# Kernel optimization log

Measured on AMD Instinct MI355X. Metric: run time of the kernel, lower is better.

The kernel has to match this reference:

```python
import jax, jax.numpy as jnp
import numpy as np

MODES1 = 64
MODES2 = 64

def _c(t):
    # real view (..., 2) -> complex
    return jax.lax.complex(t[..., 0], t[..., 1])

def _contract_tt(xf, a, b, c, d):
    # xf: (B, Cin, m1, m2) complex
    # a: (1, Cout, r1, 2), b: (r1, Cin, r2, 2), c: (r2, m1, r3, 2), d: (r3, m2, 1, 2)
    ac = _c(a)[0]          # (Cout, r1)
    bc = _c(b)             # (r1, Cin, r2)
    cc = _c(c)             # (r2, m1, r3)
    dc = _c(d)[..., 0]     # (r3, m2)
    o1 = jnp.einsum('jxk,ky,bcxy->jbcxy', cc, dc, xf)   # (r2, B, Cin, m1, m2)
    return jnp.einsum('oi,icj,jbcxy->boxy', ac, bc, o1)  # (B, Cout, m1, m2)

def setup_inputs() -> dict:
    key = jax.random.key(0)
    ks = jax.random.split(key, 9)
    std = 0.02
    inp = {
        'x':  jax.random.normal(ks[0], (4, 128, 256, 256), dtype=jnp.float32),
        'a1': std * jax.random.normal(ks[1], (1, 128, 64, 2), dtype=jnp.float32),
        'b1': std * jax.random.normal(ks[2], (64, 128, 32, 2), dtype=jnp.float32),
        'c1': std * jax.random.normal(ks[3], (32, 64, 32, 2), dtype=jnp.float32),
        'd1': std * jax.random.normal(ks[4], (32, 64, 1, 2), dtype=jnp.float32),
        'a2': std * jax.random.normal(ks[5], (1, 128, 64, 2), dtype=jnp.float32),
        'b2': std * jax.random.normal(ks[6], (64, 128, 32, 2), dtype=jnp.float32),
        'c2': std * jax.random.normal(ks[7], (32, 64, 32, 2), dtype=jnp.float32),
        'd2': std * jax.random.normal(ks[8], (32, 64, 1, 2), dtype=jnp.float32),
    }
    return inp

def reference(x, a1, b1, c1, d1, a2, b2, c2, d2):
    B, Cin, H, W = x.shape
    Cout = a1.shape[1]
    x_ft = jnp.fft.rfft2(x)  # (B, Cin, H, W//2+1) complex64
    out1 = _contract_tt(x_ft[:, :, :MODES1, :MODES2], a1, b1, c1, d1)
    out2 = _contract_tt(x_ft[:, :, -MODES1:, :MODES2], a2, b2, c2, d2)
    out_ft = jnp.zeros((B, Cout, H, W // 2 + 1), dtype=x_ft.dtype)
    out_ft = out_ft.at[:, :, :MODES1, :MODES2].set(out1)
    out_ft = out_ft.at[:, :, -MODES1:, :MODES2].set(out2)
    return jnp.fft.irfft2(out_ft, s=(H, W))
```

## Files before the change

kernel.cpp:

```cpp
#include <hip/hip_runtime.h>
#include <math.h>


#define TWO_PI 6.28318530717958647692f

typedef __attribute__((ext_vector_type(8))) short short8v;
typedef __attribute__((ext_vector_type(4))) float float4v;

namespace {
constexpr size_t P_ = 32768;

constexpr size_t oYT = 0;
constexpr size_t oTA = 1048576;
constexpr size_t oXF = 16777216;
constexpr size_t oOF = 25165824;
constexpr size_t oBF = 33554432;
constexpr size_t oAF1 = 33587200;
constexpr size_t oAF2 = 33685504;
constexpr size_t oG  = 33792000;
constexpr size_t oEF = oG + 262144;
constexpr size_t WS_FLOATS = oG + 524288;
}

__device__ __forceinline__ unsigned short f2bf(float f) {
    unsigned int u = __float_as_uint(f);
    unsigned int r = (u + 0x7FFFu + ((u >> 16) & 1u)) >> 16;
    return (unsigned short)r;
}
__device__ __forceinline__ float bf2f(unsigned short b) {
    return __uint_as_float(((unsigned int)b) << 16);
}

__global__ __launch_bounds__(256) void k_prepTables(const float* __restrict__ a1,
                                                    const float* __restrict__ a2,
                                                    unsigned short* __restrict__ AF1,
                                                    unsigned short* __restrict__ AF2,
                                                    unsigned short* __restrict__ BF,
                                                    unsigned short* __restrict__ EF,
                                                    unsigned short* __restrict__ AFa) {
    int idx = blockIdx.x * 256 + threadIdx.x;
    if (idx < 196608) {
        int tbl = (idx >= 98304);
        int id = tbl ? (idx - 98304) : idx;
        int e = id & 7, lane = (id >> 3) & 63;
        int pl = id >> 15;
        float ang;
        if (!tbl) {
            int rt = (id >> 9) & 7, kc = (id >> 12) & 7;
            int r = rt * 16 + (lane & 15);
            int s = kc * 32 + 8 * (lane >> 4) + e;
            int kh = r + ((r >= 64) ? 128 : 0);
            int ph = (kh * s) & 255;
            ang = -TWO_PI * (float)ph / 256.0f;
        } else {
            int rt = (id >> 9) & 15, kc = (id >> 13) & 3;
            int r = rt * 16 + (lane & 15);
            int s = kc * 32 + 8 * (lane >> 4) + e;
            int kh = s + ((s >= 64) ? 128 : 0);
            int ph = (kh * r) & 255;
            ang = TWO_PI * (float)ph / 256.0f;
        }
        float sn, cs; sincosf(ang, &sn, &cs);
        float v = (pl == 0) ? cs : ((pl == 1) ? sn : -sn);
        (tbl ? AF2 : AF1)[id] = f2bf(v);
    } else if (idx < 229376) {
        int id = idx - 196608;
        int e = id & 7, lane = (id >> 3) & 63;
        int nt = (id >> 9) & 3, kc = (id >> 11) & 7;
        int pl = id >> 14;
        int kw = nt * 16 + (lane & 15);
        int w = kc * 32 + 8 * (lane >> 4) + e;
        int ph = (w * kw) & 255;
        float ang = -TWO_PI * (float)ph / 256.0f;
        float sn, cs; sincosf(ang, &sn, &cs);
        BF[id] = f2bf((pl == 0) ? cs : sn);
    } else if (idx < 262144) {
        int id = idx - 229376;
        int e = id & 7, lane = (id >> 3) & 63;
        int nt = (id >> 9) & 15, kc = (id >> 13) & 1, pl = id >> 14;
        int w = nt * 16 + (lane & 15);
        int kw = kc * 32 + 8 * (lane >> 4) + e;
        int ph = (kw * w) & 255;
        float ang = TWO_PI * (float)ph / 256.0f;
        float sn, cs; sincosf(ang, &sn, &cs);
        float sc = ((kw == 0) ? 1.0f : 2.0f) / 65536.0f;
        float v = (pl == 0) ? (sc * cs) : (-sc * sn);
        EF[id] = f2bf(v);
    } else {
        int id = idx - 262144;
        int e = id & 7, lane = (id >> 3) & 63;
        int rt = (id >> 9) & 7, kc = (id >> 12) & 1;
        int plreg = id >> 13;
        int reg = plreg / 3, pl = plreg % 3;
        int o = rt * 16 + (lane & 15);
        int i = kc * 32 + 8 * (lane >> 4) + e;
        const float* ap = reg ? a2 : a1;
        float ar = ap[(o * 64 + i) * 2 + 0];
        float ai = ap[(o * 64 + i) * 2 + 1];
        float v = (pl == 0) ? ar : ((pl == 1) ? ai : -ai);
        AFa[id] = f2bf(v);
    }
}

__global__ __launch_bounds__(256) void k_g(const float* __restrict__ c1, const float* __restrict__ d1,
                                           const float* __restrict__ c2, const float* __restrict__ d2,
                                           float2* __restrict__ G) {
    int idx = blockIdx.x * 256 + threadIdx.x;
    int r = idx >> 17;
    int rem = idx & 131071;
    int j = rem >> 12;
    int xy = rem & 4095;
    int xm = xy >> 6, ym = xy & 63;
    const float* cp = r ? c2 : c1;
    const float* dp = r ? d2 : d1;
    float sr = 0.f, si = 0.f;
    for (int kk = 0; kk < 32; ++kk) {
        float cr = cp[((j * 64 + xm) * 32 + kk) * 2 + 0];
        float ci = cp[((j * 64 + xm) * 32 + kk) * 2 + 1];
        float dr = dp[(kk * 64 + ym) * 2 + 0];
        float di = dp[(kk * 64 + ym) * 2 + 1];
        sr = fmaf(cr, dr, fmaf(-ci, di, sr));
        si = fmaf(cr, di, fmaf( ci, dr, si));
    }
    G[(size_t)(r * 32 + j) * 4096 + xy] = make_float2(sr, si);
}

__global__ __launch_bounds__(256) void k_prepBG(const float* __restrict__ b1, const float* __restrict__ b2,
                                                const float2* __restrict__ G,
                                                unsigned short* __restrict__ bA,
                                                unsigned short* __restrict__ gB) {
    size_t idx = (size_t)blockIdx.x * 256 + threadIdx.x;
    if (idx < 1048576) {
        int e     = idx & 7;
        int lane  = (idx >> 3) & 63;
        int c     = (idx >> 9) & 127;
        int itile = (idx >> 16) & 3;
        int reg   = (idx >> 18) & 1;
        int plane = (idx >> 19) & 1;
        int i = itile * 16 + (lane & 15);
        int j = 8 * (lane >> 4) + e;
        const float* bp = reg ? b2 : b1;
        float v = bp[((size_t)(i * 128 + c) * 32 + j) * 2 + plane];
        bA[idx] = f2bf(v);
    } else if (idx < 1048576 + 786432) {
        size_t i2 = idx - 1048576;
        int e     = i2 & 7;
        int lane  = (i2 >> 3) & 63;
        int ytile = (i2 >> 9) & 3;
        int x     = (i2 >> 11) & 63;
        int reg   = (i2 >> 17) & 1;
        int plane = (int)(i2 >> 18);
        int y = ytile * 16 + (lane & 15);
        int j = 8 * (lane >> 4) + e;
        float2 gv = G[(size_t)(reg * 32 + j) * 4096 + x * 64 + y];
        float v = (plane == 0) ? gv.x : ((plane == 1) ? gv.y : -gv.y);
        gB[i2] = f2bf(v);
    }
}

__global__ __launch_bounds__(256) void k_stage1m(const float* __restrict__ x,
                                                 const unsigned short* __restrict__ BF,
                                                 unsigned short* __restrict__ Yt) {
    __shared__ __align__(16) unsigned short es[8192];
    int t = threadIdx.x;
    int wave = t >> 6, lane = t & 63;
    size_t row0 = (size_t)blockIdx.x * 128 + (size_t)wave * 32;
    int colp = lane & 15, rowq = lane >> 4;
    const short8v* esv = (const short8v*)es;

    float4v accR[2][4], accI[2][4];
#pragma unroll
    for (int rt = 0; rt < 2; ++rt)
#pragma unroll
        for (int nt = 0; nt < 4; ++nt) {
            accR[rt][nt] = (float4v){0.f, 0.f, 0.f, 0.f};
            accI[rt][nt] = (float4v){0.f, 0.f, 0.f, 0.f};
        }

    const float* xb0 = x + (row0 + colp) * 256 + 8 * rowq;
    const float* xb1 = xb0 + 16 * 256;
    float4 nv[2][2];
    nv[0][0] = *(const float4*)(xb0);  nv[0][1] = *(const float4*)(xb0 + 4);
    nv[1][0] = *(const float4*)(xb1);  nv[1][1] = *(const float4*)(xb1 + 4);

    const float4* bf4 = (const float4*)BF;
    for (int ph = 0; ph < 4; ++ph) {
        __syncthreads();
        {
#pragma unroll
            for (int i = 0; i < 4; ++i) {
                int idx = t + 256 * i;
                int li  = idx & 63;
                int nt  = (idx >> 6) & 3;
                int kcl = (idx >> 8) & 1;
                int pl  = idx >> 9;
                ((float4*)es)[idx] = bf4[((size_t)(pl * 8 + ph * 2 + kcl) * 4 + nt) * 64 + li];
            }
        }
        __syncthreads();
        for (int kcl = 0; kcl < 2; ++kcl) {
            int kc = ph * 2 + kcl;
            short8v xh[2];
#pragma unroll
            for (int rt = 0; rt < 2; ++rt) {
                float4 v0 = nv[rt][0], v1 = nv[rt][1];
                float vv[8] = {v0.x, v0.y, v0.z, v0.w, v1.x, v1.y, v1.z, v1.w};
#pragma unroll
                for (int j = 0; j < 8; ++j) xh[rt][j] = (short)f2bf(vv[j]);
            }
            if (kc < 7) {
                nv[0][0] = *(const float4*)(xb0 + (kc + 1) * 32);
                nv[0][1] = *(const float4*)(xb0 + (kc + 1) * 32 + 4);
                nv[1][0] = *(const float4*)(xb1 + (kc + 1) * 32);
                nv[1][1] = *(const float4*)(xb1 + (kc + 1) * 32 + 4);
            }
#pragma unroll
            for (int nt = 0; nt < 4; ++nt) {
                short8v Bch = esv[((0 * 2 + kcl) * 4 + nt) * 64 + lane];
                short8v Bsh = esv[((1 * 2 + kcl) * 4 + nt) * 64 + lane];
#pragma unroll
                for (int rt = 0; rt < 2; ++rt) {
                    accR[rt][nt] = __builtin_amdgcn_mfma_f32_16x16x32_bf16(xh[rt], Bch, accR[rt][nt], 0, 0, 0);
                    accI[rt][nt] = __builtin_amdgcn_mfma_f32_16x16x32_bf16(xh[rt], Bsh, accI[rt][nt], 0, 0, 0);
                }
            }
        }
    }

    short* Yts = (short*)Yt;
    const size_t PLY = (size_t)32 * 32768 * 8;
#pragma unroll
    for (int rt = 0; rt < 2; ++rt) {
        size_t xrow0 = row0 + rt * 16 + rowq * 4;
        int h = (int)(xrow0 & 255), bc = (int)(xrow0 >> 8);
        size_t gbase = (size_t)(h >> 3) * 32768;
        int e0 = h & 7;
#pragma unroll
        for (int nt = 0; nt < 4; ++nt) {
            size_t p = (size_t)bc * 64 + nt * 16 + colp;
            size_t off = (gbase + p) * 8 + e0;
            float4v R = accR[rt][nt], I = accI[rt][nt];
            short rh[4], ih[4];
#pragma unroll
            for (int q = 0; q < 4; ++q) {
                rh[q] = (short)f2bf(R[q]);
                ih[q] = (short)f2bf(I[q]);
            }
            *(short4*)&Yts[0 * PLY + off] = make_short4(rh[0], rh[1], rh[2], rh[3]);
            *(short4*)&Yts[1 * PLY + off] = make_short4(ih[0], ih[1], ih[2], ih[3]);
        }
    }
}

template<int S, int RT_W>
__global__ __launch_bounds__(256) void k_cmfma(const unsigned short* __restrict__ AF,
                                               const unsigned short* __restrict__ Bt,
                                               unsigned int* __restrict__ XFh) {
    constexpr int KC = S / 32;
    constexpr int SG = S / 8;
    constexpr int RTOT = RT_W * 4;
    __shared__ __align__(16) unsigned short bs[2 * SG * 16 * 8];
    int t = threadIdx.x;
    int wave = t >> 6, lane = t & 63;
    int rt0 = wave * RT_W;
    int colp = lane & 15, rowq = lane >> 4;
    const short8v* AFv = (const short8v*)AF;
    const short8v* bsv = (const short8v*)bs;
    const size_t PLA = (size_t)KC * RTOT * 64;

    for (int pt = 0; pt < 4; ++pt) {
        int p0 = blockIdx.x * 64 + pt * 16;
        __syncthreads();
        {
            const float4* src = (const float4*)Bt;
            float4* dst = (float4*)bs;
            for (int e = t; e < 2 * SG * 16; e += 256) {
                int pl = e / (SG * 16); int rem = e - pl * (SG * 16);
                int g = rem >> 4, li = rem & 15;
                dst[e] = src[((size_t)pl * SG + g) * 32768 + p0 + li];
            }
        }
        __syncthreads();
        float4v accR[RT_W], accI[RT_W];
#pragma unroll
        for (int rt = 0; rt < RT_W; ++rt) {
            accR[rt] = (float4v){0.f, 0.f, 0.f, 0.f};
            accI[rt] = (float4v){0.f, 0.f, 0.f, 0.f};
        }
#pragma unroll
        for (int kc = 0; kc < KC; ++kc) {
            int gi = kc * 4 + rowq;
            short8v Brh = bsv[((0 * SG + gi) << 4) + colp];
            short8v Bih = bsv[((1 * SG + gi) << 4) + colp];
#pragma unroll
            for (int rt = 0; rt < RT_W; ++rt) {
                size_t ab = ((size_t)kc * RTOT + rt0 + rt) * 64 + lane;
                short8v Ac  = AFv[0 * PLA + ab];
                short8v As  = AFv[1 * PLA + ab];
                short8v Ans = AFv[2 * PLA + ab];
                float4v r_ = accR[rt];
                r_ = __builtin_amdgcn_mfma_f32_16x16x32_bf16(Ac,  Brh, r_, 0, 0, 0);
                r_ = __builtin_amdgcn_mfma_f32_16x16x32_bf16(Ans, Bih, r_, 0, 0, 0);
                accR[rt] = r_;
                float4v i_ = accI[rt];
                i_ = __builtin_amdgcn_mfma_f32_16x16x32_bf16(As, Brh, i_, 0, 0, 0);
                i_ = __builtin_amdgcn_mfma_f32_16x16x32_bf16(Ac, Bih, i_, 0, 0, 0);
                accI[rt] = i_;
            }
        }
#pragma unroll
        for (int rt = 0; rt < RT_W; ++rt) {
            int rbase = (rt0 + rt) * 16 + rowq * 4;
#pragma unroll
            for (int q = 0; q < 4; ++q) {
                unsigned int pw = (unsigned int)f2bf(accR[rt][q])
                                | ((unsigned int)f2bf(accI[rt][q]) << 16);
                XFh[(size_t)(rbase + q) * P_ + p0 + colp] = pw;
            }
        }
    }
}

__global__ __launch_bounds__(256) void k_contractA(const unsigned int* __restrict__ XFh,
                                                   const unsigned short* __restrict__ bA,
                                                   const unsigned short* __restrict__ gB,
                                                   unsigned short* __restrict__ tA) {
    __shared__ __align__(16) unsigned int xfs[4][128][16];
    int t = threadIdx.x;
    int k = blockIdx.x >> 2;
    int ytile = blockIdx.x & 3;
    int y0 = ytile << 4;
    int reg = (k >= 64) ? 1 : 0;
    int x = k & 63;
    int itile = t >> 6, lane = t & 63;
    int ylane = lane & 15, qg = lane >> 4;

    {
        const uint4* src = (const uint4*)XFh;
        uint4* dst = (uint4*)xfs;
        size_t kbase = ((size_t)k * 32768 + y0) >> 2;
#pragma unroll
        for (int i = 0; i < 8; ++i) {
            int e = t + 256 * i;
            int f4w = e & 3;
            int bc  = e >> 2;
            int b   = bc >> 7, c = bc & 127;
            dst[e] = src[kbase + (size_t)b * 2048 + (size_t)c * 16 + f4w];
        }
    }

    const short8v* gBv = (const short8v*)gB;
    short8v g_r  = gBv[(((size_t)(0 * 2 + reg) * 64 + x) * 4 + ytile) * 64 + lane];
    short8v g_i  = gBv[(((size_t)(1 * 2 + reg) * 64 + x) * 4 + ytile) * 64 + lane];
    short8v g_ni = gBv[(((size_t)(2 * 2 + reg) * 64 + x) * 4 + ytile) * 64 + lane];

    const short8v* bAv = (const short8v*)bA;
    size_t aR = (((size_t)(0 * 2 + reg) * 4 + itile) * 128) * 64 + lane;
    size_t aI = (((size_t)(1 * 2 + reg) * 4 + itile) * 128) * 64 + lane;

    float tr[4][4], ti[4][4];
#pragma unroll
    for (int q = 0; q < 4; ++q)
#pragma unroll
        for (int b = 0; b < 4; ++b) { tr[q][b] = 0.f; ti[q][b] = 0.f; }

    __syncthreads();

#pragma unroll 2
    for (int c = 0; c < 128; ++c) {
        short8v av = bAv[aR + (size_t)c * 64];
        short8v aw = bAv[aI + (size_t)c * 64];
        float4v z4 = {0.f, 0.f, 0.f, 0.f};
        float4v wr = __builtin_amdgcn_mfma_f32_16x16x32_bf16(av, g_r, z4, 0, 0, 0);
        wr = __builtin_amdgcn_mfma_f32_16x16x32_bf16(aw, g_ni, wr, 0, 0, 0);
        float4v wi = __builtin_amdgcn_mfma_f32_16x16x32_bf16(av, g_i, z4, 0, 0, 0);
        wi = __builtin_amdgcn_mfma_f32_16x16x32_bf16(aw, g_r, wi, 0, 0, 0);
#pragma unroll
        for (int b = 0; b < 4; ++b) {
            unsigned int xw = xfs[b][c][ylane];
            float xr = bf2f((unsigned short)(xw & 0xFFFFu));
            float xi = bf2f((unsigned short)(xw >> 16));
#pragma unroll
            for (int q = 0; q < 4; ++q) {
                tr[q][b] = fmaf(wr[q], xr, fmaf(-wi[q], xi, tr[q][b]));
                ti[q][b] = fmaf(wr[q], xi, fmaf( wi[q], xr, ti[q][b]));
            }
        }
    }

    short* tAs = (short*)tA;
    const size_t PLT = (size_t)8 * 32768 * 8;
    int gidx = itile * 2 + (qg >> 1);
    int e0 = (qg & 1) * 4;
#pragma unroll
    for (int b = 0; b < 4; ++b) {
        size_t col = (size_t)k * 256 + (size_t)b * 64 + y0 + ylane;
        size_t off = ((size_t)gidx * 32768 + col) * 8 + e0;
        short rh[4], ih[4];
#pragma unroll
        for (int q = 0; q < 4; ++q) {
            rh[q] = (short)f2bf(tr[q][b]);
            ih[q] = (short)f2bf(ti[q][b]);
        }
        *(short4*)&tAs[0 * PLT + off] = make_short4(rh[0], rh[1], rh[2], rh[3]);
        *(short4*)&tAs[1 * PLT + off] = make_short4(ih[0], ih[1], ih[2], ih[3]);
    }
}

__global__ __launch_bounds__(256) void k_amfma(const unsigned short* __restrict__ AFa,
                                               const unsigned short* __restrict__ tA,
                                               unsigned int* __restrict__ OFh) {
    constexpr int SG = 8;
    __shared__ __align__(16) unsigned short bs[2 * SG * 16 * 8];
    int t = threadIdx.x;
    int wave = t >> 6, lane = t & 63;
    int rt0 = wave * 2;
    int colp = lane & 15, rowq = lane >> 4;
    int k = blockIdx.x >> 2, b = blockIdx.x & 3;
    int reg = (k >= 64) ? 1 : 0;
    const short8v* AFv = (const short8v*)(AFa + (size_t)reg * 3 * 2 * 8 * 512);
    const size_t PLA = 2 * 8 * 64;
    const short8v* bsv = (const short8v*)bs;
    size_t p0 = (size_t)blockIdx.x * 64;

    for (int pt = 0; pt < 4; ++pt) {
        __syncthreads();
        {
            const float4* src = (const float4*)tA;
            float4* dst = (float4*)bs;
            int e = t;
            int pl = e >> 7; int rem = e & 127;
            int g = rem >> 4, li = rem & 15;
            dst[e] = src[((size_t)pl * SG + g) * 32768 + p0 + pt * 16 + li];
        }
        __syncthreads();
        float4v accR[2], accI[2];
#pragma unroll
        for (int rt = 0; rt < 2; ++rt) {
            accR[rt] = (float4v){0.f, 0.f, 0.f, 0.f};
            accI[rt] = (float4v){0.f, 0.f, 0.f, 0.f};
        }
#pragma unroll
        for (int kc = 0; kc < 2; ++kc) {
            int gi = kc * 4 + rowq;
            short8v Brh = bsv[((0 * SG + gi) << 4) + colp];
            short8v Bih = bsv[((1 * SG + gi) << 4) + colp];
#pragma unroll
            for (int rt = 0; rt < 2; ++rt) {
                size_t ab = ((size_t)kc * 8 + rt0 + rt) * 64 + lane;
                short8v Ar  = AFv[0 * PLA + ab];
                short8v Ai  = AFv[1 * PLA + ab];
                short8v Ani = AFv[2 * PLA + ab];
                float4v r_ = accR[rt];
                r_ = __builtin_amdgcn_mfma_f32_16x16x32_bf16(Ar,  Brh, r_, 0, 0, 0);
                r_ = __builtin_amdgcn_mfma_f32_16x16x32_bf16(Ani, Bih, r_, 0, 0, 0);
                accR[rt] = r_;
                float4v i_ = accI[rt];
                i_ = __builtin_amdgcn_mfma_f32_16x16x32_bf16(Ai, Brh, i_, 0, 0, 0);
                i_ = __builtin_amdgcn_mfma_f32_16x16x32_bf16(Ar, Bih, i_, 0, 0, 0);
                accI[rt] = i_;
            }
        }
        int m = pt * 16 + colp;
#pragma unroll
        for (int rt = 0; rt < 2; ++rt) {
            int o0 = (rt0 + rt) * 16 + rowq * 4;
#pragma unroll
            for (int q = 0; q < 4; ++q) {
                unsigned int pw = (unsigned int)f2bf(accR[rt][q])
                                | ((unsigned int)f2bf(accI[rt][q]) << 16);
                OFh[(size_t)k * 32768 + (size_t)b * 8192 + (size_t)(o0 + q) * 64 + m] = pw;
            }
        }
    }
}

__global__ __launch_bounds__(512) void k_ihinv(const unsigned short* __restrict__ AF2,
                                               const unsigned int* __restrict__ OFh,
                                               const unsigned short* __restrict__ EF,
                                               float* __restrict__ out) {
    constexpr int SG = 16, KC = 4, RTOT = 16;
    __shared__ __align__(16) unsigned short zs[2 * 256 * 64];
    __shared__ __align__(16) unsigned short bs[2 * SG * 16 * 8];
    int t = threadIdx.x;
    int wave = t >> 6, lane = t & 63;
    int colp = lane & 15, rowq = lane >> 4;
    int rt0 = wave * 2;
    int bo = blockIdx.x;
    size_t p0 = (size_t)bo * 64;
    const short8v* AFv = (const short8v*)AF2;
    const short8v* bsv = (const short8v*)bs;
    const size_t PLA = (size_t)KC * RTOT * 64;

    for (int pt = 0; pt < 4; ++pt) {
        __syncthreads();
        {
            int li = t & 15, g = (t >> 4) & 15, half = t >> 8;
            int e0 = half * 4;
            short rh[4], ih[4];
#pragma unroll
            for (int j = 0; j < 4; ++j) {
                unsigned int w = OFh[(size_t)(g * 8 + e0 + j) * P_ + p0 + pt * 16 + li];
                rh[j] = (short)(w & 0xFFFFu);
                ih[j] = (short)(w >> 16);
            }
            int base = (g * 16 + li) * 8 + e0;
            *(short4*)&bs[0 * 2048 + base] = make_short4(rh[0], rh[1], rh[2], rh[3]);
            *(short4*)&bs[1 * 2048 + base] = make_short4(ih[0], ih[1], ih[2], ih[3]);
        }
        __syncthreads();
        float4v accR[2], accI[2];
#pragma unroll
        for (int rt = 0; rt < 2; ++rt) {
            accR[rt] = (float4v){0.f, 0.f, 0.f, 0.f};
            accI[rt] = (float4v){0.f, 0.f, 0.f, 0.f};
        }
#pragma unroll
        for (int kc = 0; kc < KC; ++kc) {
            int gi = kc * 4 + rowq;
            short8v Brh = bsv[((0 * SG + gi) << 4) + colp];
            short8v Bih = bsv[((1 * SG + gi) << 4) + colp];
#pragma unroll
            for (int rt = 0; rt < 2; ++rt) {
                size_t ab = ((size_t)kc * RTOT + rt0 + rt) * 64 + lane;
                short8v Ac  = AFv[0 * PLA + ab];
                short8v As  = AFv[1 * PLA + ab];
                short8v Ans = AFv[2 * PLA + ab];
                float4v r_ = accR[rt];
                r_ = __builtin_amdgcn_mfma_f32_16x16x32_bf16(Ac,  Brh, r_, 0, 0, 0);
                r_ = __builtin_amdgcn_mfma_f32_16x16x32_bf16(Ans, Bih, r_, 0, 0, 0);
                accR[rt] = r_;
                float4v i_ = accI[rt];
                i_ = __builtin_amdgcn_mfma_f32_16x16x32_bf16(As, Brh, i_, 0, 0, 0);
                i_ = __builtin_amdgcn_mfma_f32_16x16x32_bf16(Ac, Bih, i_, 0, 0, 0);
                accI[rt] = i_;
            }
        }
#pragma unroll
        for (int rt = 0; rt < 2; ++rt)
#pragma unroll
            for (int q = 0; q < 4; ++q) {
                int h = (rt0 + rt) * 16 + rowq * 4 + q;
                int kwsw = (pt * 16 + colp) ^ ((h & 7) << 3);
                zs[h * 64 + kwsw] = (unsigned short)f2bf(accR[rt][q]);
                zs[16384 + h * 64 + kwsw] = (unsigned short)f2bf(accI[rt][q]);
            }
    }
    __syncthreads();

    const short8v* EFv = (const short8v*)EF;
    for (int nt = 0; nt < 16; ++nt) {
        short8v Er0  = EFv[((0 * 2 + 0) * 16 + nt) * 64 + lane];
        short8v Er1  = EFv[((0 * 2 + 1) * 16 + nt) * 64 + lane];
        short8v nEi0 = EFv[((1 * 2 + 0) * 16 + nt) * 64 + lane];
        short8v nEi1 = EFv[((1 * 2 + 1) * 16 + nt) * 64 + lane];
#pragma unroll
        for (int mtl = 0; mtl < 2; ++mtl) {
            int h0 = (wave * 2 + mtl) * 16;
            int hA = h0 + colp;
            int sw = (hA & 7) << 3;
            short8v Zr0 = *(const short8v*)&zs[hA * 64 + ((8 * rowq) ^ sw)];
            short8v Zr1 = *(const short8v*)&zs[hA * 64 + ((32 + 8 * rowq) ^ sw)];
            short8v Zi0 = *(const short8v*)&zs[16384 + hA * 64 + ((8 * rowq) ^ sw)];
            short8v Zi1 = *(const short8v*)&zs[16384 + hA * 64 + ((32 + 8 * rowq) ^ sw)];
            float4v acc = {0.f, 0.f, 0.f, 0.f};
            acc = __builtin_amdgcn_mfma_f32_16x16x32_bf16(Zr0, Er0,  acc, 0, 0, 0);
            acc = __builtin_amdgcn_mfma_f32_16x16x32_bf16(Zi0, nEi0, acc, 0, 0, 0);
            acc = __builtin_amdgcn_mfma_f32_16x16x32_bf16(Zr1, Er1,  acc, 0, 0, 0);
            acc = __builtin_amdgcn_mfma_f32_16x16x32_bf16(Zi1, nEi1, acc, 0, 0, 0);
            size_t ob = ((size_t)bo * 256 + h0 + rowq * 4) * 256 + nt * 16 + colp;
#pragma unroll
            for (int q = 0; q < 4; ++q)
                out[ob + (size_t)q * 256] = acc[q];
        }
    }
}

extern "C" void kernel_launch(void* const* d_in, const int* in_sizes, int n_in,
                              void* d_out, int out_size, void* d_ws, size_t ws_size,
                              hipStream_t stream) {
    const float* x  = (const float*)d_in[0];
    const float* a1 = (const float*)d_in[1];
    const float* b1 = (const float*)d_in[2];
    const float* c1 = (const float*)d_in[3];
    const float* d1 = (const float*)d_in[4];
    const float* a2 = (const float*)d_in[5];
    const float* b2 = (const float*)d_in[6];
    const float* c2 = (const float*)d_in[7];
    const float* d2 = (const float*)d_in[8];
    float* out = (float*)d_out;
    float* wsf = (float*)d_ws;

    if (ws_size < WS_FLOATS * sizeof(float)) return;

    unsigned short* Yt  = (unsigned short*)(wsf + oYT);
    unsigned int*   XFh = (unsigned int*)(wsf + oXF);
    unsigned int*   OFh = (unsigned int*)(wsf + oOF);
    float2*         G   = (float2*)(wsf + oOF);
    unsigned short* BF  = (unsigned short*)(wsf + oBF);
    unsigned short* AF1 = (unsigned short*)(wsf + oAF1);
    unsigned short* AF2 = (unsigned short*)(wsf + oAF2);
    unsigned short* bA  = (unsigned short*)(wsf + oYT);
    unsigned short* gB  = bA + 1048576;
    unsigned short* tA  = (unsigned short*)(wsf + oTA);
    unsigned short* AFa = (unsigned short*)(wsf + oG);
    unsigned short* EF  = (unsigned short*)(wsf + oEF);

    k_prepTables<<<1216, 256, 0, stream>>>(a1, a2, AF1, AF2, BF, EF, AFa);
    k_g<<<1024, 256, 0, stream>>>(c1, d1, c2, d2, G);
    k_stage1m<<<1024, 256, 0, stream>>>(x, BF, Yt);
    k_cmfma<256, 2><<<512, 256, 0, stream>>>(AF1, Yt, XFh);
    k_prepBG<<<7168, 256, 0, stream>>>(b1, b2, G, bA, gB);
    k_contractA<<<512, 256, 0, stream>>>(XFh, bA, gB, tA);
    k_amfma<<<512, 256, 0, stream>>>(AFa, tA, OFh);
    k_ihinv<<<512, 512, 0, stream>>>(AF2, OFh, EF, out);

    (void)in_sizes; (void)n_in; (void)out_size;
}
```

Before: 182.7 us.

## Fuse contraction and A-factor MFMA kernels through shared memory

Merges k_contractA and k_amfma into one kernel, k_contract2. The intermediate tA tensor now stays in an LDS buffer, padded to 66 rows, instead of being written to global memory and read back. The MFMA stage then consumes it directly from LDS and writes OFh. This removes one kernel launch and a global round trip of the intermediate, at the cost of more LDS per block and more accumulator registers, which may lower occupancy.

```diff
diff --git a/kernel.cpp b/kernel.cpp
--- a/kernel.cpp
+++ b/kernel.cpp
@@ -11,7 +11,6 @@
 constexpr size_t P_ = 32768;
 
 constexpr size_t oYT = 0;
-constexpr size_t oTA = 1048576;
 constexpr size_t oXF = 16777216;
 constexpr size_t oOF = 25165824;
 constexpr size_t oBF = 33554432;
@@ -321,11 +320,13 @@
     }
 }
 
-__global__ __launch_bounds__(256) void k_contractA(const unsigned int* __restrict__ XFh,
+__global__ __launch_bounds__(256) void k_contract2(const unsigned int* __restrict__ XFh,
                                                    const unsigned short* __restrict__ bA,
                                                    const unsigned short* __restrict__ gB,
-                                                   unsigned short* __restrict__ tA) {
+                                                   const unsigned short* __restrict__ AFa,
+                                                   unsigned int* __restrict__ OFh) {
     __shared__ __align__(16) unsigned int xfs[4][128][16];
+    __shared__ __align__(16) unsigned short ts[2 * 8 * 66 * 8];
     int t = threadIdx.x;
     int k = blockIdx.x >> 2;
     int ytile = blockIdx.x & 3;
@@ -388,88 +389,73 @@
         }
     }
 
-    short* tAs = (short*)tA;
-    const size_t PLT = (size_t)8 * 32768 * 8;
-    int gidx = itile * 2 + (qg >> 1);
-    int e0 = (qg & 1) * 4;
-#pragma unroll
-    for (int b = 0; b < 4; ++b) {
-        size_t col = (size_t)k * 256 + (size_t)b * 64 + y0 + ylane;
-        size_t off = ((size_t)gidx * 32768 + col) * 8 + e0;
-        short rh[4], ih[4];
-#pragma unroll
-        for (int q = 0; q < 4; ++q) {
-            rh[q] = (short)f2bf(tr[q][b]);
-            ih[q] = (short)f2bf(ti[q][b]);
-        }
-        *(short4*)&tAs[0 * PLT + off] = make_short4(rh[0], rh[1], rh[2], rh[3]);
-        *(short4*)&tAs[1 * PLT + off] = make_short4(ih[0], ih[1], ih[2], ih[3]);
-    }
-}
-
-__global__ __launch_bounds__(256) void k_amfma(const unsigned short* __restrict__ AFa,
-                                               const unsigned short* __restrict__ tA,
-                                               unsigned int* __restrict__ OFh) {
-    constexpr int SG = 8;
-    __shared__ __align__(16) unsigned short bs[2 * SG * 16 * 8];
-    int t = threadIdx.x;
-    int wave = t >> 6, lane = t & 63;
-    int rt0 = wave * 2;
-    int colp = lane & 15, rowq = lane >> 4;
-    int k = blockIdx.x >> 2, b = blockIdx.x & 3;
-    int reg = (k >= 64) ? 1 : 0;
-    const short8v* AFv = (const short8v*)(AFa + (size_t)reg * 3 * 2 * 8 * 512);
-    const size_t PLA = 2 * 8 * 64;
-    const short8v* bsv = (const short8v*)bs;
-    size_t p0 = (size_t)blockIdx.x * 64;
-
-    for (int pt = 0; pt < 4; ++pt) {
-        __syncthreads();
-        {
-            const float4* src = (const float4*)tA;
-            float4* dst = (float4*)bs;
-            int e = t;
-            int pl = e >> 7; int rem = e & 127;
-            int g = rem >> 4, li = rem & 15;
-            dst[e] = src[((size_t)pl * SG + g) * 32768 + p0 + pt * 16 + li];
-        }
-        __syncthreads();
-        float4v accR[2], accI[2];
-#pragma unroll
-        for (int rt = 0; rt < 2; ++rt) {
-            accR[rt] = (float4v){0.f, 0.f, 0.f, 0.f};
-            accI[rt] = (float4v){0.f, 0.f, 0.f, 0.f};
-        }
-#pragma unroll
-        for (int kc = 0; kc < 2; ++kc) {
-            int gi = kc * 4 + rowq;
-            short8v Brh = bsv[((0 * SG + gi) << 4) + colp];
-            short8v Bih = bsv[((1 * SG + gi) << 4) + colp];
-#pragma unroll
-            for (int rt = 0; rt < 2; ++rt) {
-                size_t ab = ((size_t)kc * 8 + rt0 + rt) * 64 + lane;
-                short8v Ar  = AFv[0 * PLA + ab];
-                short8v Ai  = AFv[1 * PLA + ab];
-                short8v Ani = AFv[2 * PLA + ab];
-                float4v r_ = accR[rt];
-                r_ = __builtin_amdgcn_mfma_f32_16x16x32_bf16(Ar,  Brh, r_, 0, 0, 0);
-                r_ = __builtin_amdgcn_mfma_f32_16x16x32_bf16(Ani, Bih, r_, 0, 0, 0);
-                accR[rt] = r_;
-                float4v i_ = accI[rt];
-                i_ = __builtin_amdgcn_mfma_f32_16x16x32_bf16(Ai, Brh, i_, 0, 0, 0);
-                i_ = __builtin_amdgcn_mfma_f32_16x16x32_bf16(Ar, Bih, i_, 0, 0, 0);
-                accI[rt] = i_;
-            }
-        }
-        int m = pt * 16 + colp;
-#pragma unroll
-        for (int rt = 0; rt < 2; ++rt) {
-            int o0 = (rt0 + rt) * 16 + rowq * 4;
+    {
+        int gidx = itile * 2 + (qg >> 1);
+        int e0 = (qg & 1) * 4;
+#pragma unroll
+        for (int b = 0; b < 4; ++b) {
+            int n = b * 16 + ylane;
+            short rh[4], ih[4];
 #pragma unroll
             for (int q = 0; q < 4; ++q) {
-                unsigned int pw = (unsigned int)f2bf(accR[rt][q])
-                                | ((unsigned int)f2bf(accI[rt][q]) << 16);
-                OFh[(size_t)k * 32768 + (size_t)b * 8192 + (size_t)(o0 + q) * 64 + m] = pw;
+                rh[q] = (short)f2bf(tr[q][b]);
+                ih[q] = (short)f2bf(ti[q][b]);
+            }
+            *(short4*)&ts[((0 * 8 + gidx) * 66 + n) * 8 + e0] = make_short4(rh[0], rh[1], rh[2], rh[3]);
+            *(short4*)&ts[((1 * 8 + gidx) * 66 + n) * 8 + e0] = make_short4(ih[0], ih[1], ih[2], ih[3]);
+        }
+    }
+    __syncthreads();
+
+    const short8v* tsv = (const short8v*)ts;
+    const short8v* AFvE = (const short8v*)(AFa + (size_t)reg * 3 * 2 * 8 * 512);
+    const size_t PLAe = 2 * 8 * 64;
+    float4v eR[2][4], eI[2][4];
+#pragma unroll
+    for (int rtl = 0; rtl < 2; ++rtl)
+#pragma unroll
+        for (int nt = 0; nt < 4; ++nt) {
+            eR[rtl][nt] = (float4v){0.f, 0.f, 0.f, 0.f};
+            eI[rtl][nt] = (float4v){0.f, 0.f, 0.f, 0.f};
+        }
+#pragma unroll
+    for (int kc = 0; kc < 2; ++kc) {
+        int gi = kc * 4 + qg;
+        short8v Brh[4], Bih[4];
+#pragma unroll
+        for (int nt = 0; nt < 4; ++nt) {
+            Brh[nt] = tsv[(0 * 8 + gi) * 66 + nt * 16 + ylane];
+            Bih[nt] = tsv[(1 * 8 + gi) * 66 + nt * 16 + ylane];
+        }
+#pragma unroll
+        for (int rtl = 0; rtl < 2; ++rtl) {
+            size_t ab = ((size_t)kc * 8 + itile * 2 + rtl) * 64 + lane;
+            short8v Ar  = AFvE[0 * PLAe + ab];
+            short8v Ai  = AFvE[1 * PLAe + ab];
+            short8v Ani = AFvE[2 * PLAe + ab];
+#pragma unroll
+            for (int nt = 0; nt < 4; ++nt) {
+                float4v r_ = eR[rtl][nt];
+                r_ = __builtin_amdgcn_mfma_f32_16x16x32_bf16(Ar,  Brh[nt], r_, 0, 0, 0);
+                r_ = __builtin_amdgcn_mfma_f32_16x16x32_bf16(Ani, Bih[nt], r_, 0, 0, 0);
+                eR[rtl][nt] = r_;
+                float4v i_ = eI[rtl][nt];
+                i_ = __builtin_amdgcn_mfma_f32_16x16x32_bf16(Ai, Brh[nt], i_, 0, 0, 0);
+                i_ = __builtin_amdgcn_mfma_f32_16x16x32_bf16(Ar, Bih[nt], i_, 0, 0, 0);
+                eI[rtl][nt] = i_;
+            }
+        }
+    }
+#pragma unroll
+    for (int rtl = 0; rtl < 2; ++rtl) {
+        int o0 = (itile * 2 + rtl) * 16 + qg * 4;
+#pragma unroll
+        for (int nt = 0; nt < 4; ++nt) {
+#pragma unroll
+            for (int q = 0; q < 4; ++q) {
+                unsigned int pw = (unsigned int)f2bf(eR[rtl][nt][q])
+                                | ((unsigned int)f2bf(eI[rtl][nt][q]) << 16);
+                OFh[(size_t)k * 32768 + (size_t)nt * 8192 + (size_t)(o0 + q) * 64 + y0 + ylane] = pw;
             }
         }
     }
@@ -602,7 +588,6 @@
     unsigned short* AF2 = (unsigned short*)(wsf + oAF2);
     unsigned short* bA  = (unsigned short*)(wsf + oYT);
     unsigned short* gB  = bA + 1048576;
-    unsigned short* tA  = (unsigned short*)(wsf + oTA);
     unsigned short* AFa = (unsigned short*)(wsf + oG);
     unsigned short* EF  = (unsigned short*)(wsf + oEF);
 
@@ -611,8 +596,7 @@
     k_stage1m<<<1024, 256, 0, stream>>>(x, BF, Yt);
     k_cmfma<256, 2><<<512, 256, 0, stream>>>(AF1, Yt, XFh);
     k_prepBG<<<7168, 256, 0, stream>>>(b1, b2, G, bA, gB);
-    k_contractA<<<512, 256, 0, stream>>>(XFh, bA, gB, tA);
-    k_amfma<<<512, 256, 0, stream>>>(AFa, tA, OFh);
+    k_contract2<<<512, 256, 0, stream>>>(XFh, bA, gB, AFa, OFh);
     k_ihinv<<<512, 512, 0, stream>>>(AF2, OFh, EF, out);
 
     (void)in_sizes; (void)n_in; (void)out_size;
```

New measurement: 177.6 us. -2.8%, faster.
